# Optimization experiments

Hardware: AMD Instinct MI355X
Metric: run time of the kernel (lower is better)

## Reference

```python
import jax, jax.numpy as jnp
import numpy as np

N_NODES = 50000
HEADS = 16
HEAD_DIM = 8  # hidden_dim 128 / 16 heads
IN_DIM = 128
HID = HEADS * HEAD_DIM
NEG_SLOPE = 0.2


def setup_inputs() -> dict:
    key = jax.random.key(0)
    ks = jax.random.split(key, 12)
    s = 1.0 / np.sqrt(IN_DIM)
    s2 = 1.0 / np.sqrt(HID)
    return {
        "x": jax.random.normal(ks[0], (N_NODES, IN_DIM), jnp.float32),
        "edge_index": jax.random.randint(ks[1], (2, 800000), 0, N_NODES, jnp.int64),
        "W1": jax.random.normal(ks[2], (IN_DIM, HID), jnp.float32) * s,
        "a_src1": jax.random.normal(ks[3], (HEADS, HEAD_DIM), jnp.float32) * s,
        "a_dst1": jax.random.normal(ks[4], (HEADS, HEAD_DIM), jnp.float32) * s,
        "b1": jnp.zeros((HID,), jnp.float32),
        "W2": jax.random.normal(ks[5], (HID, HID), jnp.float32) * s2,
        "a_src2": jax.random.normal(ks[6], (HEADS, HEAD_DIM), jnp.float32) * s2,
        "a_dst2": jax.random.normal(ks[7], (HEADS, HEAD_DIM), jnp.float32) * s2,
        "b2": jnp.zeros((HID,), jnp.float32),
    }


def _gat_conv(x, src, dst, W, a_src, a_dst, bias):
    N = x.shape[0]
    xh = (x @ W).reshape(N, HEADS, HEAD_DIM)            # [N,H,C]
    al_s = jnp.einsum('nhc,hc->nh', xh, a_src)           # [N,H]
    al_d = jnp.einsum('nhc,hc->nh', xh, a_dst)           # [N,H]
    e = jax.nn.leaky_relu(al_s[src] + al_d[dst], NEG_SLOPE)  # [E,H]
    m = jax.ops.segment_max(e, dst, num_segments=N)      # per-dst max, [N,H]
    m = jnp.where(jnp.isfinite(m), m, 0.0)
    ex = jnp.exp(e - m[dst])
    denom = jax.ops.segment_sum(ex, dst, num_segments=N)
    alpha = ex / (denom[dst] + 1e-16)                    # [E,H]
    msg = xh[src] * alpha[:, :, None]                    # [E,H,C]
    out = jax.ops.segment_sum(msg, dst, num_segments=N)  # [N,H,C]
    return out.reshape(N, HID) + bias


def reference(x, edge_index, W1, a_src1, a_dst1, b1, W2, a_src2, a_dst2, b2):
    N = x.shape[0]
    # PyG GATConv default: add self-loops
    loops = jnp.arange(N, dtype=edge_index.dtype)
    src = jnp.concatenate([edge_index[0], loops])
    dst = jnp.concatenate([edge_index[1], loops])
    h = jax.nn.elu(_gat_conv(x, src, dst, W1, a_src1, a_dst1, b1))
    h = _gat_conv(h, src, dst, W2, a_src2, a_dst2, b2)
    return h
```

## Files before the change

### kernel.cpp

```cpp
#include <hip/hip_runtime.h>
#include <hip/hip_fp16.h>
#include <math.h>

#define DIM     128
#define HEADS   16
#define NEG     0.2f
#define GROWS   32
#define SLOTS   56
#define OVF_CAP 131072

__global__ __launch_bounds__(256) void k_gemm(const float* __restrict__ X,
                                              const float* __restrict__ W,
                                              const float* __restrict__ a_src,
                                              const float* __restrict__ a_dst,
                                              __half* __restrict__ XH16,
                                              __half* __restrict__ als16,
                                              float* __restrict__ ald,
                                              int N,
                                              int* __restrict__ zero_buf,
                                              int zero_n) {
    __shared__ float sW[DIM * DIM];
    __shared__ float sx[GROWS * DIM];
    const int t = threadIdx.x;
    const int row0 = blockIdx.x * GROWS;

    const int gid = blockIdx.x * 256 + t;
    if (zero_buf && gid < zero_n) zero_buf[gid] = 0;

    for (int i = t * 4; i < DIM * DIM; i += 256 * 4)
        *(float4*)&sW[i] = *(const float4*)&W[i];
    for (int i = t * 4; i < GROWS * DIM; i += 256 * 4) {
        const int r = row0 + (i >> 7);
        if (r < N) *(float4*)&sx[i] = *(const float4*)&X[(size_t)r * DIM + (i & 127)];
        else       *(float4*)&sx[i] = float4{0.f, 0.f, 0.f, 0.f};
    }
    __syncthreads();

    const int j0 = (t & 31) * 4;
    const int rr = (t >> 5) * 4;
    float4 a0 = {0,0,0,0}, a1 = {0,0,0,0}, a2 = {0,0,0,0}, a3 = {0,0,0,0};

    const float* sx0 = &sx[(rr + 0) * DIM];
    const float* sx1 = &sx[(rr + 1) * DIM];
    const float* sx2 = &sx[(rr + 2) * DIM];
    const float* sx3 = &sx[(rr + 3) * DIM];

#define MAC4(A, xv)                                                          \
    A.x += xv.x * w0.x + xv.y * w1.x + xv.z * w2.x + xv.w * w3.x;            \
    A.y += xv.x * w0.y + xv.y * w1.y + xv.z * w2.y + xv.w * w3.y;            \
    A.z += xv.x * w0.z + xv.y * w1.z + xv.z * w2.z + xv.w * w3.z;            \
    A.w += xv.x * w0.w + xv.y * w1.w + xv.z * w2.w + xv.w * w3.w;

#pragma unroll 4
    for (int k = 0; k < DIM; k += 4) {
        float4 x0 = *(const float4*)&sx0[k];
        float4 x1 = *(const float4*)&sx1[k];
        float4 x2 = *(const float4*)&sx2[k];
        float4 x3 = *(const float4*)&sx3[k];
        float4 w0 = *(const float4*)&sW[(k + 0) * DIM + j0];
        float4 w1 = *(const float4*)&sW[(k + 1) * DIM + j0];
        float4 w2 = *(const float4*)&sW[(k + 2) * DIM + j0];
        float4 w3 = *(const float4*)&sW[(k + 3) * DIM + j0];
        MAC4(a0, x0) MAC4(a1, x1) MAC4(a2, x2) MAC4(a3, x3)
    }
#undef MAC4

#pragma unroll
    for (int r = 0; r < 4; ++r) {
        const float4 ac = (r == 0) ? a0 : (r == 1) ? a1 : (r == 2) ? a2 : a3;
        const int row = row0 + rr + r;
        if (row < N) {
            __half2 p0 = __floats2half2_rn(ac.x, ac.y);
            __half2 p1 = __floats2half2_rn(ac.z, ac.w);
            uint2 pk;
            pk.x = *(unsigned*)&p0;
            pk.y = *(unsigned*)&p1;
            *(uint2*)&XH16[(size_t)row * DIM + j0] = pk;
        }
    }

    const int h = j0 >> 3;
    const float4 as4 = *(const float4*)&a_src[j0];
    const float4 ad4 = *(const float4*)&a_dst[j0];
#pragma unroll
    for (int r = 0; r < 4; ++r) {
        const float4 ac = (r == 0) ? a0 : (r == 1) ? a1 : (r == 2) ? a2 : a3;
        float s = ac.x * as4.x + ac.y * as4.y + ac.z * as4.z + ac.w * as4.w;
        float d = ac.x * ad4.x + ac.y * ad4.y + ac.z * ad4.z + ac.w * ad4.w;
        s += __shfl_xor(s, 1);
        d += __shfl_xor(d, 1);
        const int row = row0 + rr + r;
        if (((t & 1) == 0) && (row < N)) {
            als16[(size_t)row * HEADS + h] = __float2half_rn(s);
            ald[(size_t)row * HEADS + h]  = d;
        }
    }
}

__global__ __launch_bounds__(256) void k_fill(const void* __restrict__ ei,
                                              int* __restrict__ cnt,
                                              int* __restrict__ ovf_cnt,
                                              int* __restrict__ ssrc,
                                              int* __restrict__ ovf,
                                              int E0, int ET) {
    __shared__ int sdet;
    const int* p = (const int*)ei;
    if (threadIdx.x < 64) {
        int v = p[2 * threadIdx.x + 1];
        unsigned long long b = __ballot(v != 0);
        if (threadIdx.x == 0) sdet = (b == 0ULL) ? 1 : 0;
    }
    __syncthreads();
    const int is64 = sdet;

    const int e = blockIdx.x * 256 + threadIdx.x;
    if (e >= ET) return;
    int s, d;
    if (e < E0) {
        if (is64) {
            s = (int)((const long long*)ei)[e];
            d = (int)((const long long*)ei)[(size_t)E0 + e];
        } else {
            s = ((const int*)ei)[e];
            d = ((const int*)ei)[(size_t)E0 + e];
        }
    } else {
        s = d = e - E0;
    }
    int pz = atomicAdd(&cnt[d], 1);
    if (pz < SLOTS) {
        ssrc[(size_t)d * SLOTS + pz] = s;
    } else {
        int o = atomicAdd(ovf_cnt, 1);
        if (o < OVF_CAP) { ovf[2 * o] = s; ovf[2 * o + 1] = d; }
    }
}

__global__ __launch_bounds__(256) void k_edge(
    const int* __restrict__ cnt, const int* __restrict__ ssrc,
    const int* __restrict__ ovf, const int* __restrict__ ovf_cnt,
    const __half* __restrict__ als16, const float* __restrict__ ald,
    const __half* __restrict__ XH16, const float* __restrict__ bias,
    float* __restrict__ out, int N, int DO_ELU)
{
    const int lane = threadIdx.x & 63;
    const int node = blockIdx.x * 4 + (threadIdx.x >> 6);
    if (node >= N) return;

    const int h = lane >> 2;
    const int q = lane & 3;
    const float aldh = ald[(size_t)node * HEADS + h];
    const int dg  = cnt[node];
    const int dgS = dg < SLOTS ? dg : SLOTS;
    int myS = (lane < dgS) ? ssrc[(size_t)node * SLOTS + lane] : 0;
    const int qb = (lane & ~3) << 2;

    float acc0 = 0.f, acc1 = 0.f, sumW = 0.f;
    const int ngrp = (dgS + 3) >> 2;
    for (int g = 0; g < ngrp; ++g) {
        const int kq = 4 * g + q;
        int sL = __builtin_amdgcn_ds_bpermute(kq << 2, myS);
        float a = __half2float(als16[(size_t)sL * HEADS + h]) + aldh;
        a = (a > 0.f) ? a : NEG * a;
        float w = (kq < dgS) ? __expf(a) : 0.f;
        sumW += w;
        const int wb = __float_as_int(w);
#pragma unroll
        for (int j = 0; j < 4; ++j) {
            const int k = 4 * g + j;
            if (k >= dgS) break;
            float wj = __int_as_float(__builtin_amdgcn_ds_bpermute(qb + (j << 2), wb));
            int sj = __builtin_amdgcn_readlane(myS, k);
            float2 f = __half22float2(*(const __half2*)&XH16[(size_t)sj * DIM + 2 * lane]);
            acc0 += wj * f.x;
            acc1 += wj * f.y;
        }
    }
    sumW += __shfl_xor(sumW, 1);
    sumW += __shfl_xor(sumW, 2);

    if (dg > SLOTS) {
        int no = *ovf_cnt; if (no > OVF_CAP) no = OVF_CAP;
        for (int i = 0; i < no; ++i) {
            if (ovf[2 * i + 1] == node) {
                int os = ovf[2 * i];
                float a = __half2float(als16[(size_t)os * HEADS + h]) + aldh;
                a = (a > 0.f) ? a : NEG * a;
                float w = __expf(a);
                sumW += w;
                float2 f = __half22float2(*(const __half2*)&XH16[(size_t)os * DIM + 2 * lane]);
                acc0 += w * f.x;
                acc1 += w * f.y;
            }
        }
    }

    const float inv = 1.f / (sumW + 1e-16f);
    const float2 b2 = *(const float2*)&bias[lane * 2];
    float v0 = acc0 * inv + b2.x;
    float v1 = acc1 * inv + b2.y;
    if (DO_ELU) {
        v0 = (v0 > 0.f) ? v0 : expm1f(v0);
        v1 = (v1 > 0.f) ? v1 : expm1f(v1);
    }
    *(float2*)&out[(size_t)node * DIM + lane * 2] = float2{v0, v1};
}

extern "C" void kernel_launch(void* const* d_in, const int* in_sizes, int n_in,
                              void* d_out, int out_size, void* d_ws, size_t ws_size,
                              hipStream_t stream) {
    const float* x      = (const float*)d_in[0];
    const void*  ei     = d_in[1];
    const float* W1     = (const float*)d_in[2];
    const float* a_src1 = (const float*)d_in[3];
    const float* a_dst1 = (const float*)d_in[4];
    const float* b1     = (const float*)d_in[5];
    const float* W2     = (const float*)d_in[6];
    const float* a_src2 = (const float*)d_in[7];
    const float* a_dst2 = (const float*)d_in[8];
    const float* b2     = (const float*)d_in[9];
    float* out = (float*)d_out;

    const int N  = in_sizes[0] / DIM;
    const int E0 = in_sizes[1] / 2;
    const int ET = E0 + N;

    float*  h1      = (float*)d_ws;
    float*  ald     = h1 + (size_t)N * DIM;
    __half* xh16    = (__half*)(ald + (size_t)N * HEADS);
    __half* als16   = xh16 + (size_t)N * DIM;
    int*    cnt     = (int*)(als16 + (size_t)N * HEADS);
    int*    ovf_cnt = cnt + N;
    int*    ssrc    = ovf_cnt + 1;
    int*    ovf     = ssrc + (size_t)N * SLOTS;

    const int gemmBlocks = (N + GROWS - 1) / GROWS;
    const int edgeBlocks = (ET + 255) / 256;
    const int nodeBlocks = (N + 3) / 4;

    k_gemm<<<gemmBlocks, 256, 0, stream>>>(x, W1, a_src1, a_dst1, xh16, als16, ald, N, cnt, N + 1);
    k_fill<<<edgeBlocks, 256, 0, stream>>>(ei, cnt, ovf_cnt, ssrc, ovf, E0, ET);
    k_edge<<<nodeBlocks, 256, 0, stream>>>(cnt, ssrc, ovf, ovf_cnt, als16, ald, xh16, b1, h1, N, 1);
    k_gemm<<<gemmBlocks, 256, 0, stream>>>(h1, W2, a_src2, a_dst2, xh16, als16, ald, N, nullptr, 0);
    k_edge<<<nodeBlocks, 256, 0, stream>>>(cnt, ssrc, ovf, ovf_cnt, als16, ald, xh16, b2, out, N, 0);
}
```

Measured before the change: 373.0 us.

## Use fp16 dot2 in projection GEMM and simplify edge aggregation loop

The projection GEMM now converts W and X tiles to fp16 in shared memory, with W interleaved in k-pairs, and accumulates with packed fp16 dot2 instructions into fp32. This halves LDS footprint and load traffic and doubles math per instruction. The edge kernel drops the quad-split weight computation with ds_bpermute and instead has each lane recompute the attention weight for every neighbour directly, unrolled by 8. That removes cross-lane shuffles at the cost of redundant exp work and lower-precision GEMM inputs.

```diff
diff --git a/kernel.cpp b/kernel.cpp
--- a/kernel.cpp
+++ b/kernel.cpp
@@ -8,6 +8,21 @@
 #define GROWS   32
 #define SLOTS   56
 #define OVF_CAP 131072
+
+typedef _Float16 h2 __attribute__((ext_vector_type(2)));
+union U32H2 { unsigned u; h2 h; };
+__device__ __forceinline__ h2 u2h(unsigned u) { U32H2 x; x.u = u; return x.h; }
+__device__ __forceinline__ h2 f2h(float f) { union { float f; h2 h; } x; x.f = f; return x.h; }
+
+#if __has_builtin(__builtin_amdgcn_fdot2)
+__device__ __forceinline__ float FDOT2(h2 a, h2 b, float c) {
+    return __builtin_amdgcn_fdot2(a, b, c, false);
+}
+#else
+__device__ __forceinline__ float FDOT2(h2 a, h2 b, float c) {
+    return c + (float)a[0] * (float)b[0] + (float)a[1] * (float)b[1];
+}
+#endif
 
 __global__ __launch_bounds__(256) void k_gemm(const float* __restrict__ X,
                                               const float* __restrict__ W,
@@ -19,20 +34,34 @@
                                               int N,
                                               int* __restrict__ zero_buf,
                                               int zero_n) {
-    __shared__ float sW[DIM * DIM];
-    __shared__ float sx[GROWS * DIM];
+    __shared__ unsigned sWp[64 * DIM];
+    __shared__ __half   sx[GROWS * DIM];
     const int t = threadIdx.x;
     const int row0 = blockIdx.x * GROWS;
 
     const int gid = blockIdx.x * 256 + t;
     if (zero_buf && gid < zero_n) zero_buf[gid] = 0;
 
-    for (int i = t * 4; i < DIM * DIM; i += 256 * 4)
-        *(float4*)&sW[i] = *(const float4*)&W[i];
-    for (int i = t * 4; i < GROWS * DIM; i += 256 * 4) {
+    __half* sWh = (__half*)sWp;
+    for (int i = t * 4; i < DIM * DIM; i += 1024) {
+        float4 w = *(const float4*)&W[i];
+        const int k = i >> 7, j = i & 127;
+        const int base = ((k >> 1) * DIM) * 2 + (k & 1);
+        sWh[base + 2 * (j + 0)] = __float2half_rn(w.x);
+        sWh[base + 2 * (j + 1)] = __float2half_rn(w.y);
+        sWh[base + 2 * (j + 2)] = __float2half_rn(w.z);
+        sWh[base + 2 * (j + 3)] = __float2half_rn(w.w);
+    }
+    for (int i = t * 4; i < GROWS * DIM; i += 1024) {
         const int r = row0 + (i >> 7);
-        if (r < N) *(float4*)&sx[i] = *(const float4*)&X[(size_t)r * DIM + (i & 127)];
-        else       *(float4*)&sx[i] = float4{0.f, 0.f, 0.f, 0.f};
+        float4 v = (r < N) ? *(const float4*)&X[(size_t)r * DIM + (i & 127)]
+                           : float4{0.f, 0.f, 0.f, 0.f};
+        __half2 p0 = __floats2half2_rn(v.x, v.y);
+        __half2 p1 = __floats2half2_rn(v.z, v.w);
+        uint2 pk;
+        pk.x = *(unsigned*)&p0;
+        pk.y = *(unsigned*)&p1;
+        *(uint2*)&sx[i] = pk;
     }
     __syncthreads();
 
@@ -40,30 +69,30 @@
     const int rr = (t >> 5) * 4;
     float4 a0 = {0,0,0,0}, a1 = {0,0,0,0}, a2 = {0,0,0,0}, a3 = {0,0,0,0};
 
-    const float* sx0 = &sx[(rr + 0) * DIM];
-    const float* sx1 = &sx[(rr + 1) * DIM];
-    const float* sx2 = &sx[(rr + 2) * DIM];
-    const float* sx3 = &sx[(rr + 3) * DIM];
-
-#define MAC4(A, xv)                                                          \
-    A.x += xv.x * w0.x + xv.y * w1.x + xv.z * w2.x + xv.w * w3.x;            \
-    A.y += xv.x * w0.y + xv.y * w1.y + xv.z * w2.y + xv.w * w3.y;            \
-    A.z += xv.x * w0.z + xv.y * w1.z + xv.z * w2.z + xv.w * w3.z;            \
-    A.w += xv.x * w0.w + xv.y * w1.w + xv.z * w2.w + xv.w * w3.w;
+#define ROWDOT(A, xr)                                                         \
+    A.x = FDOT2(u2h(xr.x), u2h(w0.x), A.x); A.x = FDOT2(u2h(xr.y), u2h(w1.x), A.x); \
+    A.x = FDOT2(u2h(xr.z), u2h(w2.x), A.x); A.x = FDOT2(u2h(xr.w), u2h(w3.x), A.x); \
+    A.y = FDOT2(u2h(xr.x), u2h(w0.y), A.y); A.y = FDOT2(u2h(xr.y), u2h(w1.y), A.y); \
+    A.y = FDOT2(u2h(xr.z), u2h(w2.y), A.y); A.y = FDOT2(u2h(xr.w), u2h(w3.y), A.y); \
+    A.z = FDOT2(u2h(xr.x), u2h(w0.z), A.z); A.z = FDOT2(u2h(xr.y), u2h(w1.z), A.z); \
+    A.z = FDOT2(u2h(xr.z), u2h(w2.z), A.z); A.z = FDOT2(u2h(xr.w), u2h(w3.z), A.z); \
+    A.w = FDOT2(u2h(xr.x), u2h(w0.w), A.w); A.w = FDOT2(u2h(xr.y), u2h(w1.w), A.w); \
+    A.w = FDOT2(u2h(xr.z), u2h(w2.w), A.w); A.w = FDOT2(u2h(xr.w), u2h(w3.w), A.w);
 
 #pragma unroll 4
-    for (int k = 0; k < DIM; k += 4) {
-        float4 x0 = *(const float4*)&sx0[k];
-        float4 x1 = *(const float4*)&sx1[k];
-        float4 x2 = *(const float4*)&sx2[k];
-        float4 x3 = *(const float4*)&sx3[k];
-        float4 w0 = *(const float4*)&sW[(k + 0) * DIM + j0];
-        float4 w1 = *(const float4*)&sW[(k + 1) * DIM + j0];
-        float4 w2 = *(const float4*)&sW[(k + 2) * DIM + j0];
-        float4 w3 = *(const float4*)&sW[(k + 3) * DIM + j0];
-        MAC4(a0, x0) MAC4(a1, x1) MAC4(a2, x2) MAC4(a3, x3)
-    }
-#undef MAC4
+    for (int k8 = 0; k8 < DIM; k8 += 8) {
+        const int kp = k8 >> 1;
+        uint4 w0 = *(const uint4*)&sWp[(kp + 0) * DIM + j0];
+        uint4 w1 = *(const uint4*)&sWp[(kp + 1) * DIM + j0];
+        uint4 w2 = *(const uint4*)&sWp[(kp + 2) * DIM + j0];
+        uint4 w3 = *(const uint4*)&sWp[(kp + 3) * DIM + j0];
+        uint4 x0 = *(const uint4*)&sx[(rr + 0) * DIM + k8];
+        uint4 x1 = *(const uint4*)&sx[(rr + 1) * DIM + k8];
+        uint4 x2 = *(const uint4*)&sx[(rr + 2) * DIM + k8];
+        uint4 x3 = *(const uint4*)&sx[(rr + 3) * DIM + k8];
+        ROWDOT(a0, x0) ROWDOT(a1, x1) ROWDOT(a2, x2) ROWDOT(a3, x3)
+    }
+#undef ROWDOT
 
 #pragma unroll
     for (int r = 0; r < 4; ++r) {
@@ -148,36 +177,23 @@
     if (node >= N) return;
 
     const int h = lane >> 2;
-    const int q = lane & 3;
     const float aldh = ald[(size_t)node * HEADS + h];
     const int dg  = cnt[node];
     const int dgS = dg < SLOTS ? dg : SLOTS;
     int myS = (lane < dgS) ? ssrc[(size_t)node * SLOTS + lane] : 0;
-    const int qb = (lane & ~3) << 2;
-
-    float acc0 = 0.f, acc1 = 0.f, sumW = 0.f;
-    const int ngrp = (dgS + 3) >> 2;
-    for (int g = 0; g < ngrp; ++g) {
-        const int kq = 4 * g + q;
-        int sL = __builtin_amdgcn_ds_bpermute(kq << 2, myS);
-        float a = __half2float(als16[(size_t)sL * HEADS + h]) + aldh;
-        a = (a > 0.f) ? a : NEG * a;
-        float w = (kq < dgS) ? __expf(a) : 0.f;
-        sumW += w;
-        const int wb = __float_as_int(w);
-#pragma unroll
-        for (int j = 0; j < 4; ++j) {
-            const int k = 4 * g + j;
-            if (k >= dgS) break;
-            float wj = __int_as_float(__builtin_amdgcn_ds_bpermute(qb + (j << 2), wb));
-            int sj = __builtin_amdgcn_readlane(myS, k);
-            float2 f = __half22float2(*(const __half2*)&XH16[(size_t)sj * DIM + 2 * lane]);
-            acc0 += wj * f.x;
-            acc1 += wj * f.y;
-        }
-    }
-    sumW += __shfl_xor(sumW, 1);
-    sumW += __shfl_xor(sumW, 2);
+
+    float acc0 = 0.f, acc1 = 0.f, sum = 0.f;
+#pragma unroll 8
+    for (int k = 0; k < dgS; ++k) {
+        int s = __builtin_amdgcn_readlane(myS, k);
+        float e = __half2float(als16[(size_t)s * HEADS + h]) + aldh;
+        e = (e > 0.f) ? e : NEG * e;
+        float w = __expf(e);
+        sum += w;
+        float2 f = __half22float2(*(const __half2*)&XH16[(size_t)s * DIM + 2 * lane]);
+        acc0 += w * f.x;
+        acc1 += w * f.y;
+    }
 
     if (dg > SLOTS) {
         int no = *ovf_cnt; if (no > OVF_CAP) no = OVF_CAP;
@@ -187,7 +203,7 @@
                 float a = __half2float(als16[(size_t)os * HEADS + h]) + aldh;
                 a = (a > 0.f) ? a : NEG * a;
                 float w = __expf(a);
-                sumW += w;
+                sum += w;
                 float2 f = __half22float2(*(const __half2*)&XH16[(size_t)os * DIM + 2 * lane]);
                 acc0 += w * f.x;
                 acc1 += w * f.y;
@@ -195,7 +211,7 @@
         }
     }
 
-    const float inv = 1.f / (sumW + 1e-16f);
+    const float inv = 1.f / (sum + 1e-16f);
     const float2 b2 = *(const float2*)&bias[lane * 2];
     float v0 = acc0 * inv + b2.x;
     float v1 = acc1 * inv + b2.y;
```

After: 327.9 us. 1.14x faster.
